# Kernel tuning notes

Hardware: AMD Instinct MI355X
Metric: run time of the kernel (lower is better)

Reference implementation:

```python
import jax, jax.numpy as jnp
import numpy as np

N_NODES = 100000
N_EDGES = 600000
VOCAB = 50000
EMBED_DIM = 128
HIDDEN_DIM = 128


def gcn_conv(h, W, b, src, dst, n_nodes):
    """PyG GCNConv: x' = D^{-1/2} (A+I) D^{-1/2} X W + b.
    src/dst already include self-loops."""
    hw = h @ W                                   # [N, out]
    deg = jnp.zeros((n_nodes,), hw.dtype).at[dst].add(1.0)   # in-degree incl. self-loop
    dinv = jax.lax.rsqrt(deg)                    # deg >= 1 thanks to self-loops
    norm = dinv[src] * dinv[dst]                 # [E+N]
    msgs = norm[:, None] * hw[src]               # gather [E+N, out]
    out = jnp.zeros_like(hw).at[dst].add(msgs)   # scatter-aggregate
    return out + b


def setup_inputs() -> dict:
    key = jax.random.key(0)
    ks = jax.random.split(key, 8)
    x = jax.random.randint(ks[0], (N_NODES,), 0, VOCAB, dtype=jnp.int64 if jax.config.jax_enable_x64 else jnp.int32)
    edge_index = jax.random.randint(ks[1], (2, N_EDGES), 0, N_NODES, dtype=jnp.int32)
    emb = jax.random.normal(ks[2], (VOCAB, EMBED_DIM), dtype=jnp.float32)
    # Glorot-style scale for GCN weights
    W1 = jax.random.normal(ks[3], (EMBED_DIM, HIDDEN_DIM), dtype=jnp.float32) * (1.0 / np.sqrt(EMBED_DIM))
    b1 = jnp.zeros((HIDDEN_DIM,), dtype=jnp.float32)
    W2 = jax.random.normal(ks[4], (HIDDEN_DIM, HIDDEN_DIM), dtype=jnp.float32) * (1.0 / np.sqrt(HIDDEN_DIM))
    b2 = jnp.zeros((HIDDEN_DIM,), dtype=jnp.float32)
    return {"x": x, "edge_index": edge_index, "emb": emb, "W1": W1, "b1": b1, "W2": W2, "b2": b2}


def reference(x, edge_index, emb, W1, b1, W2, b2):
    n = x.shape[0]
    loops = jnp.arange(n, dtype=edge_index.dtype)
    src = jnp.concatenate([edge_index[0], loops])  # add self-loops once
    dst = jnp.concatenate([edge_index[1], loops])
    h = emb[x]                                     # [N, embed_dim] embedding lookup
    h = jax.nn.relu(gcn_conv(h, W1, b1, src, dst, n))
    h = jax.nn.relu(gcn_conv(h, W2, b2, src, dst, n))
    return h
```

## Files before the change

### kernel.cpp

```cpp
#include <hip/hip_runtime.h>


#define NDIM 128
#define PAD_K 136
#define SCAN_IPT 4
#define SCAN_BLK 256
#define SCAN_IPB (SCAN_BLK * SCAN_IPT)

typedef __bf16 bf16x8 __attribute__((ext_vector_type(8)));
typedef float f32x4 __attribute__((ext_vector_type(4)));

__device__ __forceinline__ float bf2f(unsigned short u) {
    union { unsigned int i; float f; } c;
    c.i = (unsigned int)u << 16;
    return c.f;
}
__device__ __forceinline__ unsigned short f2bf(float f) {
    __bf16 b = (__bf16)f;
    return __builtin_bit_cast(unsigned short, b);
}
__device__ __forceinline__ void unpack8(uint4 q, float* f) {
    f[0] = bf2f((unsigned short)(q.x & 0xffff));
    f[1] = bf2f((unsigned short)(q.x >> 16));
    f[2] = bf2f((unsigned short)(q.y & 0xffff));
    f[3] = bf2f((unsigned short)(q.y >> 16));
    f[4] = bf2f((unsigned short)(q.z & 0xffff));
    f[5] = bf2f((unsigned short)(q.z >> 16));
    f[6] = bf2f((unsigned short)(q.w & 0xffff));
    f[7] = bf2f((unsigned short)(q.w >> 16));
}

__global__ void degree_count(const int* __restrict__ dst, int* __restrict__ cnt, int E) {
    int e = blockIdx.x * blockDim.x + threadIdx.x;
    if (e < E) atomicAdd(&cnt[dst[e]], 1);
}

__global__ void scan_blocks(const int* __restrict__ in, int* __restrict__ out,
                            int* __restrict__ bsums, int n) {
    __shared__ int lds[SCAN_BLK];
    const int t = threadIdx.x;
    const int base = blockIdx.x * SCAN_IPB + t * SCAN_IPT;
    int v[SCAN_IPT];
    int s = 0;
#pragma unroll
    for (int k = 0; k < SCAN_IPT; ++k) { v[k] = (base + k < n) ? in[base + k] : 0; s += v[k]; }
    lds[t] = s;
    __syncthreads();
    for (int off = 1; off < SCAN_BLK; off <<= 1) {
        int x = (t >= off) ? lds[t - off] : 0;
        __syncthreads();
        lds[t] += x;
        __syncthreads();
    }
    if (t == SCAN_BLK - 1) bsums[blockIdx.x] = lds[t];
    int run = (t == 0) ? 0 : lds[t - 1];
#pragma unroll
    for (int k = 0; k < SCAN_IPT; ++k) {
        if (base + k < n) out[base + k] = run;
        run += v[k];
    }
}

__global__ void scan_partials(int* __restrict__ bsums, int nb) {
    __shared__ int lds[128];
    const int t = threadIdx.x;
    lds[t] = (t < nb) ? bsums[t] : 0;
    __syncthreads();
    for (int off = 1; off < 128; off <<= 1) {
        int x = (t >= off) ? lds[t - off] : 0;
        __syncthreads();
        lds[t] += x;
        __syncthreads();
    }
    if (t < nb) bsums[t] = (t == 0) ? 0 : lds[t - 1];
}

__global__ void add_offsets_dinv(int* __restrict__ rp, const int* __restrict__ bsums,
                                 const int* __restrict__ cnt, float* __restrict__ dinv, int n) {
    int i = blockIdx.x * blockDim.x + threadIdx.x;
    if (i < n) {
        rp[i] += bsums[i / SCAN_IPB];
        dinv[i] = rsqrtf((float)cnt[i] + 1.0f);
    }
}

__global__ void fill_edges(const int* __restrict__ src, const int* __restrict__ dst,
                           int* __restrict__ rp, const int* __restrict__ x,
                           const float* __restrict__ dinv,
                           int* __restrict__ esrc, int2* __restrict__ ew, int E) {
    int e = blockIdx.x * blockDim.x + threadIdx.x;
    if (e >= E) return;
    int d = dst[e], s = src[e];
    int p = atomicAdd(&rp[d], 1);
    esrc[p] = s;
    ew[p] = make_int2(x[s], __float_as_int(dinv[s]));
}

__global__ void wt_convert2(const float* __restrict__ W1, const float* __restrict__ W2,
                            unsigned short* __restrict__ WT1, unsigned short* __restrict__ WT2) {
    int c = blockIdx.x * blockDim.x + threadIdx.x;
    int cc = c & 16383;
    int j = cc >> 7, k = cc & 127;
    if (c < 16384) WT1[cc] = f2bf(W1[k * 128 + j]);
    else           WT2[cc] = f2bf(W2[k * 128 + j]);
}

template <int MODE, bool SCALE>
__global__ __launch_bounds__(256, 4)
void gemm_mfma(const void* __restrict__ Asrc, const unsigned short* __restrict__ WTb,
               const float* __restrict__ dinv, unsigned short* __restrict__ outb, int n) {
    __shared__ __bf16 sBT[128 * PAD_K];
    const int tid = threadIdx.x;
    const int rbase = blockIdx.x * 64;

    {
        const uint4* bsrc = (const uint4*)WTb;
#pragma unroll
        for (int i = 0; i < 8; ++i) {
            int c = tid + i * 256;
            int j = c >> 4, u = c & 15;
            *(uint4*)&sBT[j * PAD_K + u * 8] = bsrc[c];
        }
    }
    __syncthreads();

    const int wave = tid >> 6, lane = tid & 63;
    const int quad = lane >> 4, lrow = lane & 15;
    int arow = rbase + wave * 16 + lrow;
    if (arow >= n) arow = n - 1;

    f32x4 acc[8];
#pragma unroll
    for (int nt = 0; nt < 8; ++nt) acc[nt] = (f32x4)0.0f;

#pragma unroll
    for (int ks = 0; ks < 4; ++ks) {
        const int kb = ks * 32 + quad * 8;
        bf16x8 a;
        if (MODE == 0) {
            const float4* A4 = (const float4*)Asrc;
            float4 v0 = A4[(size_t)arow * 32 + (kb >> 2)];
            float4 v1 = A4[(size_t)arow * 32 + (kb >> 2) + 1];
            a = (bf16x8){(__bf16)v0.x, (__bf16)v0.y, (__bf16)v0.z, (__bf16)v0.w,
                         (__bf16)v1.x, (__bf16)v1.y, (__bf16)v1.z, (__bf16)v1.w};
        } else {
            a = *(const bf16x8*)((const unsigned short*)Asrc + (size_t)arow * 128 + kb);
        }
#pragma unroll
        for (int nt = 0; nt < 8; ++nt) {
            bf16x8 b = *(const bf16x8*)&sBT[(nt * 16 + lrow) * PAD_K + kb];
            acc[nt] = __builtin_amdgcn_mfma_f32_16x16x32_bf16(a, b, acc[nt], 0, 0, 0);
        }
    }

#pragma unroll
    for (int r = 0; r < 4; ++r) {
        int grow = rbase + wave * 16 + quad * 4 + r;
        if (grow < n) {
            float dsc = SCALE ? dinv[grow] : 1.0f;
            unsigned short* orow = outb + (size_t)grow * NDIM + lrow;
#pragma unroll
            for (int nt = 0; nt < 8; ++nt)
                orow[nt * 16] = f2bf(SCALE ? dsc * acc[nt][r] : acc[nt][r]);
        }
    }
}

__global__ void aggregate1(const unsigned short* __restrict__ tab, const int* __restrict__ x,
                           const int* __restrict__ rp, const int2* __restrict__ ew,
                           const float* __restrict__ dinv, const float* __restrict__ bias,
                           unsigned short* __restrict__ outb, int n) {
    int t = blockIdx.x * blockDim.x + threadIdx.x;
    int i = t >> 4, u = t & 15;
    if (i >= n) return;
    const uint4* tab4 = (const uint4*)tab;
    float di = dinv[i];
    float acc[8];
    {
        float f[8];
        unpack8(tab4[(size_t)x[i] * 16 + u], f);
#pragma unroll
        for (int k = 0; k < 8; ++k) acc[k] = di * f[k];
    }
    int j = (i == 0) ? 0 : rp[i - 1];
    const int end = rp[i];
    for (; j + 4 <= end; j += 4) {
        int2 e0 = ew[j], e1 = ew[j + 1], e2 = ew[j + 2], e3 = ew[j + 3];
        uint4 q0 = tab4[(size_t)e0.x * 16 + u];
        uint4 q1 = tab4[(size_t)e1.x * 16 + u];
        uint4 q2 = tab4[(size_t)e2.x * 16 + u];
        uint4 q3 = tab4[(size_t)e3.x * 16 + u];
        float f0[8], f1[8], f2[8], f3[8];
        unpack8(q0, f0); unpack8(q1, f1); unpack8(q2, f2); unpack8(q3, f3);
        float n0 = __int_as_float(e0.y), n1 = __int_as_float(e1.y);
        float n2 = __int_as_float(e2.y), n3 = __int_as_float(e3.y);
#pragma unroll
        for (int k = 0; k < 8; ++k) {
            float s01 = fmaf(n0, f0[k], n1 * f1[k]);
            float s23 = fmaf(n2, f2[k], n3 * f3[k]);
            acc[k] += s01 + s23;
        }
    }
    for (; j < end; ++j) {
        int2 e = ew[j];
        uint4 q = tab4[(size_t)e.x * 16 + u];
        float f[8];
        unpack8(q, f);
        float nm = __int_as_float(e.y);
#pragma unroll
        for (int k = 0; k < 8; ++k) acc[k] = fmaf(nm, f[k], acc[k]);
    }
    const float4 b0 = ((const float4*)bias)[u * 2];
    const float4 b1 = ((const float4*)bias)[u * 2 + 1];
    float r[8];
    r[0] = fmaxf(fmaf(di, acc[0], b0.x), 0.0f);
    r[1] = fmaxf(fmaf(di, acc[1], b0.y), 0.0f);
    r[2] = fmaxf(fmaf(di, acc[2], b0.z), 0.0f);
    r[3] = fmaxf(fmaf(di, acc[3], b0.w), 0.0f);
    r[4] = fmaxf(fmaf(di, acc[4], b1.x), 0.0f);
    r[5] = fmaxf(fmaf(di, acc[5], b1.y), 0.0f);
    r[6] = fmaxf(fmaf(di, acc[6], b1.z), 0.0f);
    r[7] = fmaxf(fmaf(di, acc[7], b1.w), 0.0f);
    uint4 o;
    o.x = (unsigned)f2bf(r[0]) | ((unsigned)f2bf(r[1]) << 16);
    o.y = (unsigned)f2bf(r[2]) | ((unsigned)f2bf(r[3]) << 16);
    o.z = (unsigned)f2bf(r[4]) | ((unsigned)f2bf(r[5]) << 16);
    o.w = (unsigned)f2bf(r[6]) | ((unsigned)f2bf(r[7]) << 16);
    ((uint4*)outb)[(size_t)i * 16 + u] = o;
}

__global__ void aggregate2(const unsigned short* __restrict__ vs, const int* __restrict__ rp,
                           const int* __restrict__ esrc, const float* __restrict__ dinv,
                           const float* __restrict__ bias, float* __restrict__ out, int n) {
    int t = blockIdx.x * blockDim.x + threadIdx.x;
    int i = t >> 4, u = t & 15;
    if (i >= n) return;
    const uint4* vs4 = (const uint4*)vs;
    float acc[8];
    unpack8(vs4[(size_t)i * 16 + u], acc);
    int j = (i == 0) ? 0 : rp[i - 1];
    const int end = rp[i];
    for (; j + 4 <= end; j += 4) {
        int s0 = esrc[j], s1 = esrc[j + 1], s2 = esrc[j + 2], s3 = esrc[j + 3];
        uint4 q0 = vs4[(size_t)s0 * 16 + u];
        uint4 q1 = vs4[(size_t)s1 * 16 + u];
        uint4 q2 = vs4[(size_t)s2 * 16 + u];
        uint4 q3 = vs4[(size_t)s3 * 16 + u];
        float f0[8], f1[8], f2[8], f3[8];
        unpack8(q0, f0); unpack8(q1, f1); unpack8(q2, f2); unpack8(q3, f3);
#pragma unroll
        for (int k = 0; k < 8; ++k) acc[k] += (f0[k] + f1[k]) + (f2[k] + f3[k]);
    }
    for (; j < end; ++j) {
        int s = esrc[j];
        uint4 q = vs4[(size_t)s * 16 + u];
        float f[8];
        unpack8(q, f);
#pragma unroll
        for (int k = 0; k < 8; ++k) acc[k] += f[k];
    }
    float di = dinv[i];
    const float4 b0 = ((const float4*)bias)[u * 2];
    const float4 b1 = ((const float4*)bias)[u * 2 + 1];
    float4 r0, r1;
    r0.x = fmaxf(fmaf(di, acc[0], b0.x), 0.0f);
    r0.y = fmaxf(fmaf(di, acc[1], b0.y), 0.0f);
    r0.z = fmaxf(fmaf(di, acc[2], b0.z), 0.0f);
    r0.w = fmaxf(fmaf(di, acc[3], b0.w), 0.0f);
    r1.x = fmaxf(fmaf(di, acc[4], b1.x), 0.0f);
    r1.y = fmaxf(fmaf(di, acc[5], b1.y), 0.0f);
    r1.z = fmaxf(fmaf(di, acc[6], b1.z), 0.0f);
    r1.w = fmaxf(fmaf(di, acc[7], b1.w), 0.0f);
    ((float4*)out)[(size_t)i * 32 + u * 2] = r0;
    ((float4*)out)[(size_t)i * 32 + u * 2 + 1] = r1;
}

extern "C" void kernel_launch(void* const* d_in, const int* in_sizes, int n_in,
                              void* d_out, int out_size, void* d_ws, size_t ws_size,
                              hipStream_t stream) {
    const int* x = (const int*)d_in[0];
    const int* edge_index = (const int*)d_in[1];
    const float* emb = (const float*)d_in[2];
    const float* W1 = (const float*)d_in[3];
    const float* b1 = (const float*)d_in[4];
    const float* W2 = (const float*)d_in[5];
    const float* b2 = (const float*)d_in[6];
    float* out = (float*)d_out;

    const int N = in_sizes[0];
    const int E = in_sizes[1] / 2;
    const int V = in_sizes[2] / NDIM;
    const int* src = edge_index;
    const int* dst = edge_index + E;

    char* p = (char*)d_ws;
    auto alloc = [&](size_t bytes) {
        char* q = p;
        p += (bytes + 511) & ~(size_t)511;
        return q;
    };
    int* cnt = (int*)alloc((size_t)N * sizeof(int));
    int* rp = (int*)alloc((size_t)N * sizeof(int));
    float* dinv = (float*)alloc((size_t)N * sizeof(float));
    int* bsums = (int*)alloc(128 * sizeof(int));
    int* esrc = (int*)alloc((size_t)E * sizeof(int));
    int2* ew = (int2*)alloc((size_t)E * sizeof(int2));
    unsigned short* WT1 = (unsigned short*)alloc(16384 * sizeof(unsigned short));
    unsigned short* WT2 = (unsigned short*)alloc(16384 * sizeof(unsigned short));
    unsigned short* embW1 = (unsigned short*)alloc((size_t)V * NDIM * sizeof(unsigned short));
    unsigned short* h1b = (unsigned short*)alloc((size_t)N * NDIM * sizeof(unsigned short));
    unsigned short* vs2 = (unsigned short*)alloc((size_t)N * NDIM * sizeof(unsigned short));
    (void)ws_size;

    const int NB = (N + SCAN_IPB - 1) / SCAN_IPB;

    hipMemsetAsync(cnt, 0, (size_t)N * sizeof(int), stream);
    degree_count<<<(E + 255) / 256, 256, 0, stream>>>(dst, cnt, E);
    scan_blocks<<<NB, SCAN_BLK, 0, stream>>>(cnt, rp, bsums, N);
    scan_partials<<<1, 128, 0, stream>>>(bsums, NB);
    add_offsets_dinv<<<(N + 255) / 256, 256, 0, stream>>>(rp, bsums, cnt, dinv, N);
    fill_edges<<<(E + 255) / 256, 256, 0, stream>>>(src, dst, rp, x, dinv, esrc, ew, E);

    wt_convert2<<<128, 256, 0, stream>>>(W1, W2, WT1, WT2);

    const int agg_blocks = (int)(((size_t)N * 16 + 255) / 256);

    gemm_mfma<0, false><<<(V + 63) / 64, 256, 0, stream>>>(emb, WT1, nullptr, embW1, V);
    aggregate1<<<agg_blocks, 256, 0, stream>>>(embW1, x, rp, ew, dinv, b1, h1b, N);
    gemm_mfma<1, true><<<(N + 63) / 64, 256, 0, stream>>>(h1b, WT2, dinv, vs2, N);
    aggregate2<<<agg_blocks, 256, 0, stream>>>(vs2, rp, esrc, dinv, b2, out, N);
}
```

Baseline: 247.4 us.

## Merge edge arrays into one int4 record and fuse weight conversion launch

The separate esrc and ew arrays become a single 16-byte per-edge record (src, x[src], dinv[src], pad), so fill_edges does one scattered store instead of two. Both aggregation kernels now read this record. The weight transpose/convert kernel is folded into the offset/dinv kernel as extra blocks, removing one launch, and fill_edges handles two edges per thread. In exchange, the edge array grows from 12 to 16 bytes per edge, and aggregate2 reads 16-byte records where it needs only the 4-byte src, which adds read traffic in that kernel.

```diff
diff --git a/kernel.cpp b/kernel.cpp
--- a/kernel.cpp
+++ b/kernel.cpp
@@ -75,34 +75,42 @@
     if (t < nb) bsums[t] = (t == 0) ? 0 : lds[t - 1];
 }
 
-__global__ void add_offsets_dinv(int* __restrict__ rp, const int* __restrict__ bsums,
-                                 const int* __restrict__ cnt, float* __restrict__ dinv, int n) {
-    int i = blockIdx.x * blockDim.x + threadIdx.x;
-    if (i < n) {
-        rp[i] += bsums[i / SCAN_IPB];
-        dinv[i] = rsqrtf((float)cnt[i] + 1.0f);
+__global__ void add_offsets_dinv_wt(int* __restrict__ rp, const int* __restrict__ bsums,
+                                    const int* __restrict__ cnt, float* __restrict__ dinv, int n,
+                                    int nblkA,
+                                    const float* __restrict__ W1, const float* __restrict__ W2,
+                                    unsigned short* __restrict__ WT1,
+                                    unsigned short* __restrict__ WT2) {
+    if ((int)blockIdx.x < nblkA) {
+        int i = blockIdx.x * blockDim.x + threadIdx.x;
+        if (i < n) {
+            rp[i] += bsums[i / SCAN_IPB];
+            dinv[i] = rsqrtf((float)cnt[i] + 1.0f);
+        }
+    } else {
+        int c = (blockIdx.x - nblkA) * blockDim.x + threadIdx.x;
+        int cc = c & 16383;
+        int j = cc >> 7, k = cc & 127;
+        if (c < 16384) WT1[cc] = f2bf(W1[k * 128 + j]);
+        else if (c < 32768) WT2[cc] = f2bf(W2[k * 128 + j]);
     }
 }
 
 __global__ void fill_edges(const int* __restrict__ src, const int* __restrict__ dst,
                            int* __restrict__ rp, const int* __restrict__ x,
-                           const float* __restrict__ dinv,
-                           int* __restrict__ esrc, int2* __restrict__ ew, int E) {
+                           const float* __restrict__ dinv, int4* __restrict__ ew, int E) {
+    const int stride = gridDim.x * blockDim.x;
     int e = blockIdx.x * blockDim.x + threadIdx.x;
-    if (e >= E) return;
-    int d = dst[e], s = src[e];
-    int p = atomicAdd(&rp[d], 1);
-    esrc[p] = s;
-    ew[p] = make_int2(x[s], __float_as_int(dinv[s]));
-}
-
-__global__ void wt_convert2(const float* __restrict__ W1, const float* __restrict__ W2,
-                            unsigned short* __restrict__ WT1, unsigned short* __restrict__ WT2) {
-    int c = blockIdx.x * blockDim.x + threadIdx.x;
-    int cc = c & 16383;
-    int j = cc >> 7, k = cc & 127;
-    if (c < 16384) WT1[cc] = f2bf(W1[k * 128 + j]);
-    else           WT2[cc] = f2bf(W2[k * 128 + j]);
+#pragma unroll
+    for (int k = 0; k < 2; ++k, e += stride) {
+        if (e < E) {
+            int d = dst[e], s = src[e];
+            int xs = x[s];
+            float ds = dinv[s];
+            int p = atomicAdd(&rp[d], 1);
+            ew[p] = make_int4(s, xs, __float_as_int(ds), 0);
+        }
+    }
 }
 
 template <int MODE, bool SCALE>
@@ -167,7 +175,7 @@
 }
 
 __global__ void aggregate1(const unsigned short* __restrict__ tab, const int* __restrict__ x,
-                           const int* __restrict__ rp, const int2* __restrict__ ew,
+                           const int* __restrict__ rp, const int4* __restrict__ ew,
                            const float* __restrict__ dinv, const float* __restrict__ bias,
                            unsigned short* __restrict__ outb, int n) {
     int t = blockIdx.x * blockDim.x + threadIdx.x;
@@ -185,15 +193,15 @@
     int j = (i == 0) ? 0 : rp[i - 1];
     const int end = rp[i];
     for (; j + 4 <= end; j += 4) {
-        int2 e0 = ew[j], e1 = ew[j + 1], e2 = ew[j + 2], e3 = ew[j + 3];
-        uint4 q0 = tab4[(size_t)e0.x * 16 + u];
-        uint4 q1 = tab4[(size_t)e1.x * 16 + u];
-        uint4 q2 = tab4[(size_t)e2.x * 16 + u];
-        uint4 q3 = tab4[(size_t)e3.x * 16 + u];
+        int4 e0 = ew[j], e1 = ew[j + 1], e2 = ew[j + 2], e3 = ew[j + 3];
+        uint4 q0 = tab4[(size_t)e0.y * 16 + u];
+        uint4 q1 = tab4[(size_t)e1.y * 16 + u];
+        uint4 q2 = tab4[(size_t)e2.y * 16 + u];
+        uint4 q3 = tab4[(size_t)e3.y * 16 + u];
         float f0[8], f1[8], f2[8], f3[8];
         unpack8(q0, f0); unpack8(q1, f1); unpack8(q2, f2); unpack8(q3, f3);
-        float n0 = __int_as_float(e0.y), n1 = __int_as_float(e1.y);
-        float n2 = __int_as_float(e2.y), n3 = __int_as_float(e3.y);
+        float n0 = __int_as_float(e0.z), n1 = __int_as_float(e1.z);
+        float n2 = __int_as_float(e2.z), n3 = __int_as_float(e3.z);
 #pragma unroll
         for (int k = 0; k < 8; ++k) {
             float s01 = fmaf(n0, f0[k], n1 * f1[k]);
@@ -202,11 +210,11 @@
         }
     }
     for (; j < end; ++j) {
-        int2 e = ew[j];
-        uint4 q = tab4[(size_t)e.x * 16 + u];
+        int4 e = ew[j];
+        uint4 q = tab4[(size_t)e.y * 16 + u];
         float f[8];
         unpack8(q, f);
-        float nm = __int_as_float(e.y);
+        float nm = __int_as_float(e.z);
 #pragma unroll
         for (int k = 0; k < 8; ++k) acc[k] = fmaf(nm, f[k], acc[k]);
     }
@@ -230,7 +238,7 @@
 }
 
 __global__ void aggregate2(const unsigned short* __restrict__ vs, const int* __restrict__ rp,
-                           const int* __restrict__ esrc, const float* __restrict__ dinv,
+                           const int4* __restrict__ ew, const float* __restrict__ dinv,
                            const float* __restrict__ bias, float* __restrict__ out, int n) {
     int t = blockIdx.x * blockDim.x + threadIdx.x;
     int i = t >> 4, u = t & 15;
@@ -241,7 +249,7 @@
     int j = (i == 0) ? 0 : rp[i - 1];
     const int end = rp[i];
     for (; j + 4 <= end; j += 4) {
-        int s0 = esrc[j], s1 = esrc[j + 1], s2 = esrc[j + 2], s3 = esrc[j + 3];
+        int s0 = ew[j].x, s1 = ew[j + 1].x, s2 = ew[j + 2].x, s3 = ew[j + 3].x;
         uint4 q0 = vs4[(size_t)s0 * 16 + u];
         uint4 q1 = vs4[(size_t)s1 * 16 + u];
         uint4 q2 = vs4[(size_t)s2 * 16 + u];
@@ -252,7 +260,7 @@
         for (int k = 0; k < 8; ++k) acc[k] += (f0[k] + f1[k]) + (f2[k] + f3[k]);
     }
     for (; j < end; ++j) {
-        int s = esrc[j];
+        int s = ew[j].x;
         uint4 q = vs4[(size_t)s * 16 + u];
         float f[8];
         unpack8(q, f);
@@ -303,8 +311,7 @@
     int* rp = (int*)alloc((size_t)N * sizeof(int));
     float* dinv = (float*)alloc((size_t)N * sizeof(float));
     int* bsums = (int*)alloc(128 * sizeof(int));
-    int* esrc = (int*)alloc((size_t)E * sizeof(int));
-    int2* ew = (int2*)alloc((size_t)E * sizeof(int2));
+    int4* ew = (int4*)alloc((size_t)E * sizeof(int4));
     unsigned short* WT1 = (unsigned short*)alloc(16384 * sizeof(unsigned short));
     unsigned short* WT2 = (unsigned short*)alloc(16384 * sizeof(unsigned short));
     unsigned short* embW1 = (unsigned short*)alloc((size_t)V * NDIM * sizeof(unsigned short));
@@ -313,20 +320,20 @@
     (void)ws_size;
 
     const int NB = (N + SCAN_IPB - 1) / SCAN_IPB;
+    const int nblkA = (N + 255) / 256;
 
     hipMemsetAsync(cnt, 0, (size_t)N * sizeof(int), stream);
     degree_count<<<(E + 255) / 256, 256, 0, stream>>>(dst, cnt, E);
     scan_blocks<<<NB, SCAN_BLK, 0, stream>>>(cnt, rp, bsums, N);
     scan_partials<<<1, 128, 0, stream>>>(bsums, NB);
-    add_offsets_dinv<<<(N + 255) / 256, 256, 0, stream>>>(rp, bsums, cnt, dinv, N);
-    fill_edges<<<(E + 255) / 256, 256, 0, stream>>>(src, dst, rp, x, dinv, esrc, ew, E);
-
-    wt_convert2<<<128, 256, 0, stream>>>(W1, W2, WT1, WT2);
+    add_offsets_dinv_wt<<<nblkA + 128, 256, 0, stream>>>(rp, bsums, cnt, dinv, N, nblkA,
+                                                         W1, W2, WT1, WT2);
+    fill_edges<<<(E / 2 + 255) / 256, 256, 0, stream>>>(src, dst, rp, x, dinv, ew, E);
 
     const int agg_blocks = (int)(((size_t)N * 16 + 255) / 256);
 
     gemm_mfma<0, false><<<(V + 63) / 64, 256, 0, stream>>>(emb, WT1, nullptr, embW1, V);
     aggregate1<<<agg_blocks, 256, 0, stream>>>(embW1, x, rp, ew, dinv, b1, h1b, N);
     gemm_mfma<1, true><<<(N + 63) / 64, 256, 0, stream>>>(h1b, WT2, dinv, vs2, N);
-    aggregate2<<<agg_blocks, 256, 0, stream>>>(vs2, rp, esrc, dinv, b2, out, N);
-}
+    aggregate2<<<agg_blocks, 256, 0, stream>>>(vs2, rp, ew, dinv, b2, out, N);
+}
```

New measurement: 242.2 us. 2.1% less time.
